# Optimization experiments

Measured on AMD Instinct MI355X. Metric: run time of the kernel, lower is better.

## Reference

```python
import jax, jax.numpy as jnp
import numpy as np
from jax import lax

NUM_IMG, NUM_HID, NUM_OUT = 3, 16, 10
NC = NUM_IMG + NUM_HID + NUM_OUT  # 29
HIDDEN = 128
FIRE_RATE = 0.5
LEAK = 0.01  # nn.LeakyReLU default negative_slope

_sobel_x = np.outer([1, 2, 1], [-1, 0, 1]) / 8.0
_sobel_y = _sobel_x.T

def _dw_kernel(k2d):
    # depthwise kernel, OIHW with feature_group_count=NC -> (NC, 1, 3, 3)
    k = jnp.asarray(k2d, dtype=jnp.float32)
    return jnp.tile(k[None, None], (NC, 1, 1, 1))

KSX = _dw_kernel(_sobel_x)
KSY = _dw_kernel(_sobel_y)

def _dwconv(x, k):
    # x: [B, NC, H, W]; zero padding=1 (F.conv2d default), groups=NC
    return lax.conv_general_dilated(x, k, window_strides=(1, 1),
                                    padding=((1, 1), (1, 1)),
                                    feature_group_count=NC,
                                    dimension_numbers=('NCHW', 'OIHW', 'NCHW'))

def _leaky(h):
    return jnp.where(h >= 0, h, LEAK * h)

def setup_inputs() -> dict:
    key = jax.random.key(0)
    k1, k2, k3, k4, kx = jax.random.split(key, 5)
    B, H, W = 16, 64, 64
    in_vec = NC * 3 + 1  # 29 channels x (identity + 2 sobel) + temporal = 88
    x = jax.random.uniform(kx, (B, NUM_IMG, H, W), dtype=jnp.float32)
    w1 = jax.random.normal(k1, (2 * HIDDEN, in_vec), dtype=jnp.float32) * 0.05
    b1 = jax.random.normal(k2, (2 * HIDDEN,), dtype=jnp.float32) * 0.05
    w2 = jax.random.normal(k3, (HIDDEN, 2 * HIDDEN), dtype=jnp.float32) * 0.05
    w3 = jax.random.normal(k4, (NC, HIDDEN), dtype=jnp.float32) * 0.02
    return {"x": x, "w1": w1, "b1": b1, "w2": w2, "w3": w3, "steps": 20}

def _nca_forward(x, w1, b1, w2, w3, steps):
    B, _, H, W = x.shape
    base_key = jax.random.key(42)
    # pad_input: zeros in hidden+output channels, then Gaussian noise N(0.5, 0.225) in hidden
    hid = 0.5 + 0.225 * jax.random.normal(jax.random.fold_in(base_key, 10_000),
                                          (B, NUM_HID, H, W), dtype=x.dtype)
    out = jnp.zeros((B, NUM_OUT, H, W), dtype=x.dtype)
    state = jnp.concatenate([x, hid, out], axis=1)  # [B, 29, H, W]
    # immutable image channels: zero dx on first NUM_IMG channels
    chan_mask = jnp.concatenate([jnp.zeros((NUM_IMG,), x.dtype),
                                 jnp.ones((NC - NUM_IMG,), x.dtype)])

    def step_fn(s, step):
        sx = _dwconv(s, KSX)
        sy = _dwconv(s, KSY)
        t = jnp.full((B, 1, H, W), 1.0, dtype=s.dtype) * (step.astype(s.dtype) / 100.0)
        perc = jnp.concatenate([s, sx, sy, t], axis=1)        # [B, 88, H, W]
        p = perc.transpose(0, 2, 3, 1)                         # [B, H, W, 88]
        h = _leaky(jnp.einsum('bhwi,oi->bhwo', p, w1) + b1)    # [B, H, W, 256]
        h = _leaky(jnp.einsum('bhwi,oi->bhwo', h, w2))         # [B, H, W, 128]
        dx = jnp.einsum('bhwi,oi->bhwo', h, w3)                # [B, H, W, 29]
        fire = jax.random.uniform(jax.random.fold_in(base_key, step),
                                  (B, H, W, 1), dtype=s.dtype) < FIRE_RATE
        dx = dx * fire.astype(s.dtype) * chan_mask             # stochastic + immutable mask
        s = s + dx.transpose(0, 3, 1, 2)
        return s, None

    state, _ = lax.scan(step_fn, state, jnp.arange(steps))
    # classify: mean-pool class channels over space, softmax
    class_ch = state[:, NUM_IMG + NUM_HID:, :, :]              # [B, 10, H, W]
    logits = jnp.mean(class_ch, axis=(2, 3))                   # [B, 10]
    return jax.nn.softmax(logits, axis=-1)

def reference(x, w1, b1, w2, w3, steps):
    return _nca_forward(x, w1, b1, w2, w3, steps)
```

## Files before the change

### kernel.cpp

```cpp
#include <hip/hip_runtime.h>


#define ROTL32(x, d) (((x) << (d)) | ((x) >> (32 - (d))))

struct U2 { unsigned a, b; };

__host__ __device__ inline U2 tf2x32(unsigned k0, unsigned k1, unsigned c0, unsigned c1) {
  unsigned ks2 = k0 ^ k1 ^ 0x1BD11BDAu;
  unsigned x0 = c0 + k0;
  unsigned x1 = c1 + k1;
#define TF_ROUND4(r0, r1, r2, r3)                                              \
  x0 += x1; x1 = ROTL32(x1, r0); x1 ^= x0;                                     \
  x0 += x1; x1 = ROTL32(x1, r1); x1 ^= x0;                                     \
  x0 += x1; x1 = ROTL32(x1, r2); x1 ^= x0;                                     \
  x0 += x1; x1 = ROTL32(x1, r3); x1 ^= x0;
  TF_ROUND4(13, 15, 26, 6)
  x0 += k1;  x1 += ks2 + 1u;
  TF_ROUND4(17, 29, 16, 24)
  x0 += ks2; x1 += k0 + 2u;
  TF_ROUND4(13, 15, 26, 6)
  x0 += k0;  x1 += k1 + 3u;
  TF_ROUND4(17, 29, 16, 24)
  x0 += k1;  x1 += ks2 + 4u;
  TF_ROUND4(13, 15, 26, 6)
  x0 += ks2; x1 += k0 + 5u;
#undef TF_ROUND4
  U2 r; r.a = x0; r.b = x1; return r;
}

__device__ inline float erfinv_xla(float x) {
  float w = -log1pf(-x * x);
  float p;
  if (w < 5.0f) {
    w -= 2.5f;
    p = 2.81022636e-08f;
    p = fmaf(p, w, 3.43273939e-07f);
    p = fmaf(p, w, -3.5233877e-06f);
    p = fmaf(p, w, -4.39150654e-06f);
    p = fmaf(p, w, 0.00021858087f);
    p = fmaf(p, w, -0.00125372503f);
    p = fmaf(p, w, -0.00417768164f);
    p = fmaf(p, w, 0.246640727f);
    p = fmaf(p, w, 1.50140941f);
  } else {
    w = sqrtf(w) - 3.0f;
    p = -0.000200214257f;
    p = fmaf(p, w, 0.000100950558f);
    p = fmaf(p, w, 0.00134934322f);
    p = fmaf(p, w, -0.00367342844f);
    p = fmaf(p, w, 0.00573950773f);
    p = fmaf(p, w, -0.0076224613f);
    p = fmaf(p, w, 0.00943887047f);
    p = fmaf(p, w, 1.00167406f);
    p = fmaf(p, w, 2.83297682f);
  }
  return p * x;
}

__device__ inline float leaky(float v) { return fmaxf(v, 0.01f * v); }

typedef __attribute__((ext_vector_type(8))) short bf16x8;
typedef __attribute__((ext_vector_type(4))) float f32x4;
typedef __attribute__((ext_vector_type(4))) unsigned int u32x4;

__host__ __device__ inline unsigned short bf16_rne(float x) {
  unsigned u = __float_as_uint(x);
  return (unsigned short)((u + 0x7FFFu + ((u >> 16) & 1u)) >> 16);
}

__device__ inline unsigned cvtpk(float a, float b) {
  unsigned r;
  asm("v_cvt_pk_bf16_f32 %0, %1, %2" : "=v"(r) : "v"(a), "v"(b));
  return r;
}

union Frag8 { u32x4 u; bf16x8 v; };

__device__ inline void split8(const float v[8], bf16x8& hi, bf16x8& lo) {
  Frag8 H, L;
#pragma unroll
  for (int j = 0; j < 8; j += 2) {
    unsigned p = cvtpk(v[j], v[j + 1]);
    H.u[j >> 1] = p;
    float r0 = v[j]     - __uint_as_float(p << 16);
    float r1 = v[j + 1] - __uint_as_float(p & 0xFFFF0000u);
    L.u[j >> 1] = cvtpk(r0, r1);
  }
  hi = H.v;
  lo = L.v;
}

__device__ inline int swz64(int m, int off) {
  int g = (off >> 4) ^ (m & 3);
  return (g << 4) | (off & 15);
}
__device__ inline int swz256(int m, int off) {
  int g = off >> 4;
  g = (g & ~7) | ((g ^ (m & 7)) & 7);
  return (g << 4) | (off & 15);
}

#define MFMA(a, b, c) __builtin_amdgcn_mfma_f32_16x16x32_bf16((a), (b), (c), 0, 0, 0)

__global__ void prep_weights(const float* __restrict__ w1, const float* __restrict__ w2,
                             const float* __restrict__ w3,
                             unsigned short* __restrict__ pw1,
                             unsigned short* __restrict__ pw2,
                             unsigned short* __restrict__ pw3) {
  int i = blockIdx.x * 256 + threadIdx.x;
  int e = i & 511, L = e >> 3, j = e & 7;
  int kq = (L >> 4) * 8 + j;
  int ln = L & 15;
  if (i < 96 * 512) {
    int tile = i >> 9;
    int f = tile & 3, kc = (tile >> 2) % 3, nc = tile / 12;
    int n = nc * 32 + (f >> 1) * 16 + ln;
    int src;
    if (kc == 0)      src = (kq < 29) ? kq : -1;
    else if (kc == 1) src = (kq < 29) ? 29 + kq : ((kq == 29) ? 87 : -1);
    else              src = (kq < 29) ? 58 + kq : -1;
    float v = (src >= 0) ? w1[n * 88 + src] : 0.0f;
    unsigned short h = bf16_rne(v);
    pw1[i] = (f & 1) ? bf16_rne(v - __uint_as_float(((unsigned)h) << 16)) : h;
  }
  if (i < 128 * 512) {
    int tile = i >> 9;
    int hl = tile & 1, t = (tile >> 1) & 7, nc = tile >> 4;
    int n = t * 16 + ln;
    int k = nc * 32 + kq;
    float v = w2[n * 256 + k];
    unsigned short h = bf16_rne(v);
    pw2[i] = hl ? bf16_rne(v - __uint_as_float(((unsigned)h) << 16)) : h;
  }
  if (i < 16 * 512) {
    int tile = i >> 9;
    int f = tile & 3, kc = tile >> 2;
    int n = (f >> 1) * 16 + ln;
    int k = kc * 32 + kq;
    float v = (n < 29) ? w3[n * 128 + k] : 0.0f;
    unsigned short h = bf16_rne(v);
    pw3[i] = (f & 1) ? bf16_rne(v - __uint_as_float(((unsigned)h) << 16)) : h;
  }
}

__global__ void init_state(const float* __restrict__ x, float* __restrict__ s0,
                           float* __restrict__ s1, unsigned hk0, unsigned hk1) {
  int idx = blockIdx.x * 256 + threadIdx.x;
  if (idx >= 16 * 29 * 4096) return;
  int pix = idx & 4095;
  int c = (idx >> 12) % 29;
  int b = idx / (4096 * 29);
  float v;
  if (c < 3) {
    v = x[(b * 3 + c) * 4096 + pix];
    s1[idx] = v;
  } else if (c < 19) {
    int ch = c - 3;
    int i = (b * 16 + ch) * 4096 + pix;
    const int half = 131072;
    unsigned bits;
    if (i < half) bits = tf2x32(hk0, hk1, (unsigned)i, (unsigned)(i + half)).a;
    else          bits = tf2x32(hk0, hk1, (unsigned)(i - half), (unsigned)i).b;
    float f = __uint_as_float((bits >> 9) | 0x3F800000u) - 1.0f;
    const float lo = -0x1.fffffep-1f;
    float u = fmaxf(lo, fmaf(f, 2.0f, lo));
    v = fmaf(0.225f, 1.41421356237f * erfinv_xla(u), 0.5f);
  } else {
    v = 0.0f;
  }
  s0[idx] = v;
}

__global__ __launch_bounds__(256, 2) void nca_step(
    const float* __restrict__ sin_, float* __restrict__ sout,
    const unsigned short* __restrict__ pw1, const float* __restrict__ b1,
    const unsigned short* __restrict__ pw2, const unsigned short* __restrict__ pw3,
    float tval, unsigned fk0, unsigned fk1) {
  __shared__ __align__(16) char lds[81920];
  char* h1h = lds;
  char* h1l = lds + 8192;
  char* h2h = lds + 16384;
  char* h2l = lds + 49152;
  float* sS = (float*)(lds + 16384);

  const int tid = threadIdx.x;
  const int w = tid >> 6;
  const int L = tid & 63;
  const int lane16 = L & 15;
  const int quad = L >> 4;
  const int b = blockIdx.z;
  const int ty0 = blockIdx.y * 8;
  const int tx0 = blockIdx.x * 16;
  const float* sb = sin_ + b * 29 * 4096;

  {
    float hv[21];
    int hix[21];
#pragma unroll
    for (int it = 0; it < 21; ++it) {
      int l = tid + it * 256;
      int c = l / 180;
      int rem = l - c * 180;
      int r = rem / 18;
      int x = rem - r * 18;
      int gy = ty0 - 1 + r, gx = tx0 - 1 + x;
      bool in = (l < 29 * 180);
      float v = 0.0f;
      if (in && (unsigned)gy < 64u && (unsigned)gx < 64u)
        v = sb[c * 4096 + gy * 64 + gx];
      hv[it] = v;
      hix[it] = in ? (c * 181 + r * 18 + x) : 5249;
    }
#pragma unroll
    for (int it = 0; it < 21; ++it) sS[hix[it]] = hv[it];
  }
  __syncthreads();

  const int am0 = w * 32 + lane16;
  const int am1 = w * 32 + 16 + lane16;
  bf16x8 a1h[2][3], a1l[2][3];
#pragma unroll
  for (int tt = 0; tt < 2; ++tt) {
    float vps[8], vpx[8], vpy[8];
#pragma unroll
    for (int j = 0; j < 8; ++j) {
      int c = quad * 8 + j;
      int cc = (c < 29) ? c : 0;
      const float* S = sS + cc * 181 + (2 * w + tt + 1) * 18 + (lane16 + 1);
      float m00 = S[-19], m01 = S[-18], m02 = S[-17];
      float m10 = S[-1],  m11 = S[0],   m12 = S[1];
      float m20 = S[17],  m21 = S[18],  m22 = S[19];
      bool valid = (c < 29);
      vps[j] = valid ? m11 : 0.0f;
      float px = ((m02 - m00) + 2.0f * (m12 - m10) + (m22 - m20)) * 0.125f;
      float py = ((m20 + 2.0f * m21 + m22) - (m00 + 2.0f * m01 + m02)) * 0.125f;
      vpx[j] = valid ? px : ((c == 29) ? tval : 0.0f);
      vpy[j] = valid ? py : 0.0f;
    }
    split8(vps, a1h[tt][0], a1l[tt][0]);
    split8(vpx, a1h[tt][1], a1l[tt][1]);
    split8(vpy, a1h[tt][2], a1l[tt][2]);
  }
  __syncthreads();

  const int L16 = L * 16;

  bf16x8 n1a, n1b, n1c, n1d;
  {
    const char* g = (const char*)pw1;
    n1a = *(const bf16x8*)(g + L16);
    n1b = *(const bf16x8*)(g + 1024 + L16);
    n1c = *(const bf16x8*)(g + 2048 + L16);
    n1d = *(const bf16x8*)(g + 3072 + L16);
  }

  float fire0, fire1;
  {
    int i0 = b * 4096 + (ty0 + 2 * w) * 64 + (tx0 + lane16);
    unsigned bits;
    if (i0 < 32768) bits = tf2x32(fk0, fk1, (unsigned)i0, (unsigned)(i0 + 32768)).a;
    else            bits = tf2x32(fk0, fk1, (unsigned)(i0 - 32768), (unsigned)i0).b;
    fire0 = (bits & 0x80000000u) ? 0.0f : 1.0f;
    int i1 = i0 + 64;
    if (i1 < 32768) bits = tf2x32(fk0, fk1, (unsigned)i1, (unsigned)(i1 + 32768)).a;
    else            bits = tf2x32(fk0, fk1, (unsigned)(i1 - 32768), (unsigned)i1).b;
    fire1 = (bits & 0x80000000u) ? 0.0f : 1.0f;
  }

  f32x4 acc2a[8], acc2b[8];
#pragma unroll
  for (int t = 0; t < 8; ++t) {
    acc2a[t] = (f32x4){0.f, 0.f, 0.f, 0.f};
    acc2b[t] = (f32x4){0.f, 0.f, 0.f, 0.f};
  }

#pragma unroll 1
  for (int nc = 0; nc < 8; ++nc) {
    f32x4 c0a = (f32x4){0.f, 0.f, 0.f, 0.f};
    f32x4 c1a = (f32x4){0.f, 0.f, 0.f, 0.f};
    f32x4 c0b = (f32x4){0.f, 0.f, 0.f, 0.f};
    f32x4 c1b = (f32x4){0.f, 0.f, 0.f, 0.f};
#pragma unroll
    for (int kc = 0; kc < 3; ++kc) {
      bf16x8 w1a = n1a, w1b = n1b, w1cc = n1c, w1d = n1d;
      {
        const int nt = (kc < 2) ? (nc * 3 + kc + 1) : (((nc + 1) & 7) * 3);
        const char* g = (const char*)pw1 + nt * 4096;
        n1a = *(const bf16x8*)(g + L16);
        n1b = *(const bf16x8*)(g + 1024 + L16);
        n1c = *(const bf16x8*)(g + 2048 + L16);
        n1d = *(const bf16x8*)(g + 3072 + L16);
      }
      __builtin_amdgcn_s_setprio(1);
      c0a = MFMA(a1h[0][kc], w1a, c0a);
      c1a = MFMA(a1h[0][kc], w1cc, c1a);
      c0b = MFMA(a1h[1][kc], w1a, c0b);
      c1b = MFMA(a1h[1][kc], w1cc, c1b);
      c0a = MFMA(a1h[0][kc], w1b, c0a);
      c1a = MFMA(a1h[0][kc], w1d, c1a);
      c0b = MFMA(a1h[1][kc], w1b, c0b);
      c1b = MFMA(a1h[1][kc], w1d, c1b);
      c0a = MFMA(a1l[0][kc], w1a, c0a);
      c1a = MFMA(a1l[0][kc], w1cc, c1a);
      c0b = MFMA(a1l[1][kc], w1a, c0b);
      c1b = MFMA(a1l[1][kc], w1cc, c1b);
      __builtin_amdgcn_s_setprio(0);
    }

    const char* g2 = (const char*)pw2 + nc * 16384;
    bf16x8 p0h = *(const bf16x8*)(g2 + L16);
    bf16x8 p0l = *(const bf16x8*)(g2 + 1024 + L16);
    bf16x8 p1h = *(const bf16x8*)(g2 + 2048 + L16);
    bf16x8 p1l = *(const bf16x8*)(g2 + 3072 + L16);

    float bv0 = b1[nc * 32 + lane16];
    float bv1 = b1[nc * 32 + 16 + lane16];
#pragma unroll
    for (int tt = 0; tt < 2; ++tt) {
      f32x4 cc0 = tt ? c0b : c0a;
      f32x4 cc1 = tt ? c1b : c1a;
#pragma unroll
      for (int r = 0; r < 4; ++r) {
        int m = w * 32 + tt * 16 + quad * 4 + r;
        float v0 = leaky(cc0[r] + bv0);
        float v1 = leaky(cc1[r] + bv1);
        unsigned ph = cvtpk(v0, v1);
        float r0 = v0 - __uint_as_float(ph << 16);
        float r1 = v1 - __uint_as_float(ph & 0xFFFF0000u);
        unsigned pl = cvtpk(r0, r1);
        *(unsigned short*)(h1h + m * 64 + swz64(m, lane16 * 2)) = (unsigned short)ph;
        *(unsigned short*)(h1h + m * 64 + swz64(m, 32 + lane16 * 2)) = (unsigned short)(ph >> 16);
        *(unsigned short*)(h1l + m * 64 + swz64(m, lane16 * 2)) = (unsigned short)pl;
        *(unsigned short*)(h1l + m * 64 + swz64(m, 32 + lane16 * 2)) = (unsigned short)(pl >> 16);
      }
    }
    bf16x8 ah0 = *(const bf16x8*)(h1h + am0 * 64 + swz64(am0, quad * 16));
    bf16x8 al0 = *(const bf16x8*)(h1l + am0 * 64 + swz64(am0, quad * 16));
    bf16x8 ah1 = *(const bf16x8*)(h1h + am1 * 64 + swz64(am1, quad * 16));
    bf16x8 al1 = *(const bf16x8*)(h1l + am1 * 64 + swz64(am1, quad * 16));
#pragma unroll
    for (int t = 0; t < 8; ++t) {
      bf16x8 bh = (t & 1) ? p1h : p0h;
      bf16x8 bl = (t & 1) ? p1l : p0l;
      if (t < 6) {
        const char* g = g2 + (t + 2) * 2048;
        if (t & 1) {
          p1h = *(const bf16x8*)(g + L16);
          p1l = *(const bf16x8*)(g + 1024 + L16);
        } else {
          p0h = *(const bf16x8*)(g + L16);
          p0l = *(const bf16x8*)(g + 1024 + L16);
        }
      }
      __builtin_amdgcn_s_setprio(1);
      acc2a[t] = MFMA(ah0, bh, acc2a[t]);
      acc2b[t] = MFMA(ah1, bh, acc2b[t]);
      acc2a[t] = MFMA(ah0, bl, acc2a[t]);
      acc2b[t] = MFMA(ah1, bl, acc2b[t]);
      acc2a[t] = MFMA(al0, bh, acc2a[t]);
      acc2b[t] = MFMA(al1, bh, acc2b[t]);
      __builtin_amdgcn_s_setprio(0);
    }
  }

#pragma unroll
  for (int tt = 0; tt < 2; ++tt) {
#pragma unroll
    for (int t = 0; t < 8; t += 2) {
#pragma unroll
      for (int r = 0; r < 4; ++r) {
        int m = w * 32 + tt * 16 + quad * 4 + r;
        float va = leaky(tt ? acc2b[t][r] : acc2a[t][r]);
        float vb = leaky(tt ? acc2b[t + 1][r] : acc2a[t + 1][r]);
        unsigned ph = cvtpk(va, vb);
        float ra = va - __uint_as_float(ph << 16);
        float rb = vb - __uint_as_float(ph & 0xFFFF0000u);
        unsigned pl = cvtpk(ra, rb);
        int offa = (t * 16 + lane16) * 2;
        int offb = ((t + 1) * 16 + lane16) * 2;
        *(unsigned short*)(h2h + m * 256 + swz256(m, offa)) = (unsigned short)ph;
        *(unsigned short*)(h2h + m * 256 + swz256(m, offb)) = (unsigned short)(ph >> 16);
        *(unsigned short*)(h2l + m * 256 + swz256(m, offa)) = (unsigned short)pl;
        *(unsigned short*)(h2l + m * 256 + swz256(m, offb)) = (unsigned short)(pl >> 16);
      }
    }
  }

  bf16x8 m0, m1, m2, m3;
  {
    const char* g = (const char*)pw3;
    m0 = *(const bf16x8*)(g + L16);
    m1 = *(const bf16x8*)(g + 1024 + L16);
    m2 = *(const bf16x8*)(g + 2048 + L16);
    m3 = *(const bf16x8*)(g + 3072 + L16);
  }
  f32x4 d0a = (f32x4){0.f, 0.f, 0.f, 0.f};
  f32x4 d1a = (f32x4){0.f, 0.f, 0.f, 0.f};
  f32x4 d0b = (f32x4){0.f, 0.f, 0.f, 0.f};
  f32x4 d1b = (f32x4){0.f, 0.f, 0.f, 0.f};
#pragma unroll
  for (int kc = 0; kc < 4; ++kc) {
    bf16x8 q0 = m0, q1 = m1, q2 = m2, q3 = m3;
    if (kc < 3) {
      const char* g = (const char*)pw3 + (kc + 1) * 4096;
      m0 = *(const bf16x8*)(g + L16);
      m1 = *(const bf16x8*)(g + 1024 + L16);
      m2 = *(const bf16x8*)(g + 2048 + L16);
      m3 = *(const bf16x8*)(g + 3072 + L16);
    }
    bf16x8 ah0 = *(const bf16x8*)(h2h + am0 * 256 + swz256(am0, kc * 64 + quad * 16));
    bf16x8 al0 = *(const bf16x8*)(h2l + am0 * 256 + swz256(am0, kc * 64 + quad * 16));
    bf16x8 ah1 = *(const bf16x8*)(h2h + am1 * 256 + swz256(am1, kc * 64 + quad * 16));
    bf16x8 al1 = *(const bf16x8*)(h2l + am1 * 256 + swz256(am1, kc * 64 + quad * 16));
    __builtin_amdgcn_s_setprio(1);
    d0a = MFMA(ah0, q0, d0a);
    d1a = MFMA(ah0, q2, d1a);
    d0b = MFMA(ah1, q0, d0b);
    d1b = MFMA(ah1, q2, d1b);
    d0a = MFMA(ah0, q1, d0a);
    d1a = MFMA(ah0, q3, d1a);
    d0b = MFMA(ah1, q1, d0b);
    d1b = MFMA(ah1, q3, d1b);
    d0a = MFMA(al0, q0, d0a);
    d1a = MFMA(al0, q2, d1a);
    d0b = MFMA(al1, q0, d0b);
    d1b = MFMA(al1, q2, d1b);
    __builtin_amdgcn_s_setprio(0);
  }

  float fr0[4], fr1[4];
#pragma unroll
  for (int r = 0; r < 4; ++r) {
    fr0[r] = __shfl(fire0, quad * 4 + r, 64);
    fr1[r] = __shfl(fire1, quad * 4 + r, 64);
  }
  int gxq = tx0 + quad * 4;
  float* ob = sout + b * 29 * 4096;
#pragma unroll
  for (int tt = 0; tt < 2; ++tt) {
    int gy = ty0 + 2 * w + tt;
#pragma unroll
    for (int t3 = 0; t3 < 2; ++t3) {
      int c = t3 * 16 + lane16;
      if (c >= 3 && c <= 28) {
        float4 so = *(const float4*)(sb + c * 4096 + gy * 64 + gxq);
        f32x4 d = tt ? (t3 ? d1b : d0b) : (t3 ? d1a : d0a);
        const float* fr = tt ? fr1 : fr0;
        float4 o;
        o.x = fmaf(fr[0], d[0], so.x);
        o.y = fmaf(fr[1], d[1], so.y);
        o.z = fmaf(fr[2], d[2], so.z);
        o.w = fmaf(fr[3], d[3], so.w);
        *(float4*)(ob + c * 4096 + gy * 64 + gxq) = o;
      }
    }
  }
}

__global__ __launch_bounds__(256) void reduce_ch(const float* __restrict__ s,
                                                 float* __restrict__ part) {
  int blk = blockIdx.x;
  int b = blk / 10, o = blk - b * 10;
  const float4* ch = (const float4*)(s + ((size_t)b * 29 + 19 + o) * 4096);
  int tid = threadIdx.x;
  float4 v0 = ch[tid];
  float4 v1 = ch[tid + 256];
  float4 v2 = ch[tid + 512];
  float4 v3 = ch[tid + 768];
  float p = ((v0.x + v0.y) + (v0.z + v0.w)) + ((v1.x + v1.y) + (v1.z + v1.w)) +
            ((v2.x + v2.y) + (v2.z + v2.w)) + ((v3.x + v3.y) + (v3.z + v3.w));
#pragma unroll
  for (int d = 32; d > 0; d >>= 1) p += __shfl_down(p, d, 64);
  __shared__ float red[4];
  if ((tid & 63) == 0) red[tid >> 6] = p;
  __syncthreads();
  if (tid == 0)
    part[blk] = ((red[0] + red[1]) + (red[2] + red[3])) * (1.0f / 4096.0f);
}

__global__ __launch_bounds__(64) void softmax10(const float* __restrict__ part,
                                                float* __restrict__ out) {
  int b = blockIdx.x;
  int o = threadIdx.x;
  float v = (o < 10) ? part[b * 10 + o] : -__builtin_inff();
  float m = v;
#pragma unroll
  for (int d = 8; d > 0; d >>= 1) m = fmaxf(m, __shfl_xor(m, d, 16));
  float e = (o < 10) ? __expf(v - m) : 0.0f;
  e = (o < 10) ? expf(v - m) : 0.0f;
  float sum = e;
#pragma unroll
  for (int d = 8; d > 0; d >>= 1) sum += __shfl_xor(sum, d, 16);
  if (o < 10) out[b * 10 + o] = e / sum;
}

extern "C" void kernel_launch(void* const* d_in, const int* in_sizes, int n_in,
                              void* d_out, int out_size, void* d_ws, size_t ws_size,
                              hipStream_t stream) {
  const float* x  = (const float*)d_in[0];
  const float* w1 = (const float*)d_in[1];
  const float* b1 = (const float*)d_in[2];
  const float* w2 = (const float*)d_in[3];
  const float* w3 = (const float*)d_in[4];
  const int STEPS = 20;

  const size_t STATE = (size_t)16 * 29 * 4096;
  float* ws = (float*)d_ws;
  float* s0 = ws;
  float* s1 = ws + STATE;
  unsigned short* pw1 = (unsigned short*)(ws + 2 * STATE);
  unsigned short* pw2 = pw1 + 96 * 512;
  unsigned short* pw3 = pw2 + 128 * 512;
  float* part = (float*)(pw3 + 16 * 512);
  (void)ws_size; (void)n_in; (void)in_sizes; (void)out_size;

  prep_weights<<<256, 256, 0, stream>>>(w1, w2, w3, pw1, pw2, pw3);

  U2 hk = tf2x32(0u, 42u, 0u, 10000u);
  init_state<<<(16 * 29 * 4096 + 255) / 256, 256, 0, stream>>>(x, s0, s1, hk.a, hk.b);

  for (int s = 0; s < STEPS; ++s) {
    U2 fk = tf2x32(0u, 42u, 0u, (unsigned)s);
    float tval = (float)s / 100.0f;
    const float* in = (s & 1) ? s1 : s0;
    float* out = (s & 1) ? s0 : s1;
    dim3 grid(4, 8, 16);
    nca_step<<<grid, 256, 0, stream>>>(in, out, pw1, b1, pw2, pw3, tval, fk.a, fk.b);
  }
  reduce_ch<<<160, 256, 0, stream>>>(s0, part);
  softmax10<<<16, 64, 0, stream>>>(part, (float*)d_out);
}
```

Before: 692.5 us.

## Double per-block tile to 16x16 pixels to amortize weight loads over more rows

Each block now processes a 16x16 pixel tile (4 row-tiles per wave instead of 2), so weight fragments loaded from global memory feed twice as many MFMAs. LDS grows to 128KB and launch bounds drop to one block per CU, and the grid halves to 256 blocks. This trades occupancy and halo overhead for more weight reuse, and it raises register pressure with 32 accumulator tiles per wave.

After: 843.3 us. 21.8% more time.

```diff
diff --git a/kernel.cpp b/kernel.cpp
--- a/kernel.cpp
+++ b/kernel.cpp
@@ -171,17 +171,17 @@
   s0[idx] = v;
 }
 
-__global__ __launch_bounds__(256, 2) void nca_step(
+__global__ __launch_bounds__(256, 1) void nca_step(
     const float* __restrict__ sin_, float* __restrict__ sout,
     const unsigned short* __restrict__ pw1, const float* __restrict__ b1,
     const unsigned short* __restrict__ pw2, const unsigned short* __restrict__ pw3,
     float tval, unsigned fk0, unsigned fk1) {
-  __shared__ __align__(16) char lds[81920];
-  char* h1h = lds;
-  char* h1l = lds + 8192;
-  char* h2h = lds + 16384;
-  char* h2l = lds + 49152;
-  float* sS = (float*)(lds + 16384);
+  __shared__ __align__(16) char lds[131072];
+  char* h2h = lds;
+  char* h2l = lds + 65536;
+  char* h1h = lds + 65536;
+  char* h1l = lds + 65536 + 16384;
+  float* sS = (float*)lds;
 
   const int tid = threadIdx.x;
   const int w = tid >> 6;
@@ -189,44 +189,63 @@
   const int lane16 = L & 15;
   const int quad = L >> 4;
   const int b = blockIdx.z;
-  const int ty0 = blockIdx.y * 8;
+  const int ty0 = blockIdx.y * 16;
   const int tx0 = blockIdx.x * 16;
   const float* sb = sin_ + b * 29 * 4096;
 
   {
-    float hv[21];
-    int hix[21];
-#pragma unroll
-    for (int it = 0; it < 21; ++it) {
+    float hv[19];
+    int hix[19];
+#pragma unroll
+    for (int it = 0; it < 19; ++it) {
       int l = tid + it * 256;
-      int c = l / 180;
-      int rem = l - c * 180;
+      int c = l / 324;
+      int rem = l - c * 324;
       int r = rem / 18;
       int x = rem - r * 18;
       int gy = ty0 - 1 + r, gx = tx0 - 1 + x;
-      bool in = (l < 29 * 180);
+      bool in = (l < 29 * 324);
       float v = 0.0f;
       if (in && (unsigned)gy < 64u && (unsigned)gx < 64u)
         v = sb[c * 4096 + gy * 64 + gx];
       hv[it] = v;
-      hix[it] = in ? (c * 181 + r * 18 + x) : 5249;
-    }
-#pragma unroll
-    for (int it = 0; it < 21; ++it) sS[hix[it]] = hv[it];
+      hix[it] = in ? (c * 325 + r * 18 + x) : 9425;
+    }
+#pragma unroll
+    for (int it = 0; it < 19; ++it) sS[hix[it]] = hv[it];
+  }
+  {
+    float hv[18];
+    int hix[18];
+#pragma unroll
+    for (int it = 0; it < 18; ++it) {
+      int l = tid + (19 + it) * 256;
+      int c = l / 324;
+      int rem = l - c * 324;
+      int r = rem / 18;
+      int x = rem - r * 18;
+      int gy = ty0 - 1 + r, gx = tx0 - 1 + x;
+      bool in = (l < 29 * 324);
+      float v = 0.0f;
+      if (in && (unsigned)gy < 64u && (unsigned)gx < 64u)
+        v = sb[c * 4096 + gy * 64 + gx];
+      hv[it] = v;
+      hix[it] = in ? (c * 325 + r * 18 + x) : 9425;
+    }
+#pragma unroll
+    for (int it = 0; it < 18; ++it) sS[hix[it]] = hv[it];
   }
   __syncthreads();
 
-  const int am0 = w * 32 + lane16;
-  const int am1 = w * 32 + 16 + lane16;
-  bf16x8 a1h[2][3], a1l[2][3];
-#pragma unroll
-  for (int tt = 0; tt < 2; ++tt) {
+  bf16x8 a1h[4][3], a1l[4][3];
+#pragma unroll
+  for (int tt = 0; tt < 4; ++tt) {
     float vps[8], vpx[8], vpy[8];
 #pragma unroll
     for (int j = 0; j < 8; ++j) {
       int c = quad * 8 + j;
       int cc = (c < 29) ? c : 0;
-      const float* S = sS + cc * 181 + (2 * w + tt + 1) * 18 + (lane16 + 1);
+      const float* S = sS + cc * 325 + (4 * w + tt + 1) * 18 + (lane16 + 1);
       float m00 = S[-19], m01 = S[-18], m02 = S[-17];
       float m10 = S[-1],  m11 = S[0],   m12 = S[1];
       float m20 = S[17],  m21 = S[18],  m22 = S[19];
@@ -244,6 +263,7 @@
   __syncthreads();
 
   const int L16 = L * 16;
+  const int am0 = w * 64 + lane16;
 
   bf16x8 n1a, n1b, n1c, n1d;
   {
@@ -254,32 +274,30 @@
     n1d = *(const bf16x8*)(g + 3072 + L16);
   }
 
-  float fire0, fire1;
-  {
-    int i0 = b * 4096 + (ty0 + 2 * w) * 64 + (tx0 + lane16);
+  float fire[4];
+#pragma unroll
+  for (int tt = 0; tt < 4; ++tt) {
+    int i = b * 4096 + (ty0 + 4 * w + tt) * 64 + (tx0 + lane16);
     unsigned bits;
-    if (i0 < 32768) bits = tf2x32(fk0, fk1, (unsigned)i0, (unsigned)(i0 + 32768)).a;
-    else            bits = tf2x32(fk0, fk1, (unsigned)(i0 - 32768), (unsigned)i0).b;
-    fire0 = (bits & 0x80000000u) ? 0.0f : 1.0f;
-    int i1 = i0 + 64;
-    if (i1 < 32768) bits = tf2x32(fk0, fk1, (unsigned)i1, (unsigned)(i1 + 32768)).a;
-    else            bits = tf2x32(fk0, fk1, (unsigned)(i1 - 32768), (unsigned)i1).b;
-    fire1 = (bits & 0x80000000u) ? 0.0f : 1.0f;
-  }
-
-  f32x4 acc2a[8], acc2b[8];
-#pragma unroll
-  for (int t = 0; t < 8; ++t) {
-    acc2a[t] = (f32x4){0.f, 0.f, 0.f, 0.f};
-    acc2b[t] = (f32x4){0.f, 0.f, 0.f, 0.f};
-  }
+    if (i < 32768) bits = tf2x32(fk0, fk1, (unsigned)i, (unsigned)(i + 32768)).a;
+    else           bits = tf2x32(fk0, fk1, (unsigned)(i - 32768), (unsigned)i).b;
+    fire[tt] = (bits & 0x80000000u) ? 0.0f : 1.0f;
+  }
+
+  f32x4 acc2[4][8];
+#pragma unroll
+  for (int tt = 0; tt < 4; ++tt)
+#pragma unroll
+    for (int t = 0; t < 8; ++t) acc2[tt][t] = (f32x4){0.f, 0.f, 0.f, 0.f};
 
 #pragma unroll 1
   for (int nc = 0; nc < 8; ++nc) {
-    f32x4 c0a = (f32x4){0.f, 0.f, 0.f, 0.f};
-    f32x4 c1a = (f32x4){0.f, 0.f, 0.f, 0.f};
-    f32x4 c0b = (f32x4){0.f, 0.f, 0.f, 0.f};
-    f32x4 c1b = (f32x4){0.f, 0.f, 0.f, 0.f};
+    f32x4 c0[4], c1[4];
+#pragma unroll
+    for (int tt = 0; tt < 4; ++tt) {
+      c0[tt] = (f32x4){0.f, 0.f, 0.f, 0.f};
+      c1[tt] = (f32x4){0.f, 0.f, 0.f, 0.f};
+    }
 #pragma unroll
     for (int kc = 0; kc < 3; ++kc) {
       bf16x8 w1a = n1a, w1b = n1b, w1cc = n1c, w1d = n1d;
@@ -292,18 +310,21 @@
         n1d = *(const bf16x8*)(g + 3072 + L16);
       }
       __builtin_amdgcn_s_setprio(1);
-      c0a = MFMA(a1h[0][kc], w1a, c0a);
-      c1a = MFMA(a1h[0][kc], w1cc, c1a);
-      c0b = MFMA(a1h[1][kc], w1a, c0b);
-      c1b = MFMA(a1h[1][kc], w1cc, c1b);
-      c0a = MFMA(a1h[0][kc], w1b, c0a);
-      c1a = MFMA(a1h[0][kc], w1d, c1a);
-      c0b = MFMA(a1h[1][kc], w1b, c0b);
-      c1b = MFMA(a1h[1][kc], w1d, c1b);
-      c0a = MFMA(a1l[0][kc], w1a, c0a);
-      c1a = MFMA(a1l[0][kc], w1cc, c1a);
-      c0b = MFMA(a1l[1][kc], w1a, c0b);
-      c1b = MFMA(a1l[1][kc], w1cc, c1b);
+#pragma unroll
+      for (int tt = 0; tt < 4; ++tt) {
+        c0[tt] = MFMA(a1h[tt][kc], w1a, c0[tt]);
+        c1[tt] = MFMA(a1h[tt][kc], w1cc, c1[tt]);
+      }
+#pragma unroll
+      for (int tt = 0; tt < 4; ++tt) {
+        c0[tt] = MFMA(a1h[tt][kc], w1b, c0[tt]);
+        c1[tt] = MFMA(a1h[tt][kc], w1d, c1[tt]);
+      }
+#pragma unroll
+      for (int tt = 0; tt < 4; ++tt) {
+        c0[tt] = MFMA(a1l[tt][kc], w1a, c0[tt]);
+        c1[tt] = MFMA(a1l[tt][kc], w1cc, c1[tt]);
+      }
       __builtin_amdgcn_s_setprio(0);
     }
 
@@ -316,14 +337,12 @@
     float bv0 = b1[nc * 32 + lane16];
     float bv1 = b1[nc * 32 + 16 + lane16];
 #pragma unroll
-    for (int tt = 0; tt < 2; ++tt) {
-      f32x4 cc0 = tt ? c0b : c0a;
-      f32x4 cc1 = tt ? c1b : c1a;
+    for (int tt = 0; tt < 4; ++tt) {
 #pragma unroll
       for (int r = 0; r < 4; ++r) {
-        int m = w * 32 + tt * 16 + quad * 4 + r;
-        float v0 = leaky(cc0[r] + bv0);
-        float v1 = leaky(cc1[r] + bv1);
+        int m = w * 64 + tt * 16 + quad * 4 + r;
+        float v0 = leaky(c0[tt][r] + bv0);
+        float v1 = leaky(c1[tt][r] + bv1);
         unsigned ph = cvtpk(v0, v1);
         float r0 = v0 - __uint_as_float(ph << 16);
         float r1 = v1 - __uint_as_float(ph & 0xFFFF0000u);
@@ -334,10 +353,13 @@
         *(unsigned short*)(h1l + m * 64 + swz64(m, 32 + lane16 * 2)) = (unsigned short)(pl >> 16);
       }
     }
-    bf16x8 ah0 = *(const bf16x8*)(h1h + am0 * 64 + swz64(am0, quad * 16));
-    bf16x8 al0 = *(const bf16x8*)(h1l + am0 * 64 + swz64(am0, quad * 16));
-    bf16x8 ah1 = *(const bf16x8*)(h1h + am1 * 64 + swz64(am1, quad * 16));
-    bf16x8 al1 = *(const bf16x8*)(h1l + am1 * 64 + swz64(am1, quad * 16));
+    bf16x8 ah[4], al[4];
+#pragma unroll
+    for (int tt = 0; tt < 4; ++tt) {
+      int am = am0 + tt * 16;
+      ah[tt] = *(const bf16x8*)(h1h + am * 64 + swz64(am, quad * 16));
+      al[tt] = *(const bf16x8*)(h1l + am * 64 + swz64(am, quad * 16));
+    }
 #pragma unroll
     for (int t = 0; t < 8; ++t) {
       bf16x8 bh = (t & 1) ? p1h : p0h;
@@ -353,25 +375,27 @@
         }
       }
       __builtin_amdgcn_s_setprio(1);
-      acc2a[t] = MFMA(ah0, bh, acc2a[t]);
-      acc2b[t] = MFMA(ah1, bh, acc2b[t]);
-      acc2a[t] = MFMA(ah0, bl, acc2a[t]);
-      acc2b[t] = MFMA(ah1, bl, acc2b[t]);
-      acc2a[t] = MFMA(al0, bh, acc2a[t]);
-      acc2b[t] = MFMA(al1, bh, acc2b[t]);
+#pragma unroll
+      for (int tt = 0; tt < 4; ++tt) acc2[tt][t] = MFMA(ah[tt], bh, acc2[tt][t]);
+#pragma unroll
+      for (int tt = 0; tt < 4; ++tt) acc2[tt][t] = MFMA(ah[tt], bl, acc2[tt][t]);
+#pragma unroll
+      for (int tt = 0; tt < 4; ++tt) acc2[tt][t] = MFMA(al[tt], bh, acc2[tt][t]);
       __builtin_amdgcn_s_setprio(0);
     }
   }
 
-#pragma unroll
-  for (int tt = 0; tt < 2; ++tt) {
+  __syncthreads();
+
+#pragma unroll
+  for (int tt = 0; tt < 4; ++tt) {
 #pragma unroll
     for (int t = 0; t < 8; t += 2) {
 #pragma unroll
       for (int r = 0; r < 4; ++r) {
-        int m = w * 32 + tt * 16 + quad * 4 + r;
-        float va = leaky(tt ? acc2b[t][r] : acc2a[t][r]);
-        float vb = leaky(tt ? acc2b[t + 1][r] : acc2a[t + 1][r]);
+        int m = w * 64 + tt * 16 + quad * 4 + r;
+        float va = leaky(acc2[tt][t][r]);
+        float vb = leaky(acc2[tt][t + 1][r]);
         unsigned ph = cvtpk(va, vb);
         float ra = va - __uint_as_float(ph << 16);
         float rb = vb - __uint_as_float(ph & 0xFFFF0000u);
@@ -394,10 +418,12 @@
     m2 = *(const bf16x8*)(g + 2048 + L16);
     m3 = *(const bf16x8*)(g + 3072 + L16);
   }
-  f32x4 d0a = (f32x4){0.f, 0.f, 0.f, 0.f};
-  f32x4 d1a = (f32x4){0.f, 0.f, 0.f, 0.f};
-  f32x4 d0b = (f32x4){0.f, 0.f, 0.f, 0.f};
-  f32x4 d1b = (f32x4){0.f, 0.f, 0.f, 0.f};
+  f32x4 d0[4], d1[4];
+#pragma unroll
+  for (int tt = 0; tt < 4; ++tt) {
+    d0[tt] = (f32x4){0.f, 0.f, 0.f, 0.f};
+    d1[tt] = (f32x4){0.f, 0.f, 0.f, 0.f};
+  }
 #pragma unroll
   for (int kc = 0; kc < 4; ++kc) {
     bf16x8 q0 = m0, q1 = m1, q2 = m2, q3 = m3;
@@ -408,44 +434,46 @@
       m2 = *(const bf16x8*)(g + 2048 + L16);
       m3 = *(const bf16x8*)(g + 3072 + L16);
     }
-    bf16x8 ah0 = *(const bf16x8*)(h2h + am0 * 256 + swz256(am0, kc * 64 + quad * 16));
-    bf16x8 al0 = *(const bf16x8*)(h2l + am0 * 256 + swz256(am0, kc * 64 + quad * 16));
-    bf16x8 ah1 = *(const bf16x8*)(h2h + am1 * 256 + swz256(am1, kc * 64 + quad * 16));
-    bf16x8 al1 = *(const bf16x8*)(h2l + am1 * 256 + swz256(am1, kc * 64 + quad * 16));
+    bf16x8 ah[4], al[4];
+#pragma unroll
+    for (int tt = 0; tt < 4; ++tt) {
+      int am = am0 + tt * 16;
+      ah[tt] = *(const bf16x8*)(h2h + am * 256 + swz256(am, kc * 64 + quad * 16));
+      al[tt] = *(const bf16x8*)(h2l + am * 256 + swz256(am, kc * 64 + quad * 16));
+    }
     __builtin_amdgcn_s_setprio(1);
-    d0a = MFMA(ah0, q0, d0a);
-    d1a = MFMA(ah0, q2, d1a);
-    d0b = MFMA(ah1, q0, d0b);
-    d1b = MFMA(ah1, q2, d1b);
-    d0a = MFMA(ah0, q1, d0a);
-    d1a = MFMA(ah0, q3, d1a);
-    d0b = MFMA(ah1, q1, d0b);
-    d1b = MFMA(ah1, q3, d1b);
-    d0a = MFMA(al0, q0, d0a);
-    d1a = MFMA(al0, q2, d1a);
-    d0b = MFMA(al1, q0, d0b);
-    d1b = MFMA(al1, q2, d1b);
+#pragma unroll
+    for (int tt = 0; tt < 4; ++tt) {
+      d0[tt] = MFMA(ah[tt], q0, d0[tt]);
+      d1[tt] = MFMA(ah[tt], q2, d1[tt]);
+    }
+#pragma unroll
+    for (int tt = 0; tt < 4; ++tt) {
+      d0[tt] = MFMA(ah[tt], q1, d0[tt]);
+      d1[tt] = MFMA(ah[tt], q3, d1[tt]);
+    }
+#pragma unroll
+    for (int tt = 0; tt < 4; ++tt) {
+      d0[tt] = MFMA(al[tt], q0, d0[tt]);
+      d1[tt] = MFMA(al[tt], q2, d1[tt]);
+    }
     __builtin_amdgcn_s_setprio(0);
   }
 
-  float fr0[4], fr1[4];
-#pragma unroll
-  for (int r = 0; r < 4; ++r) {
-    fr0[r] = __shfl(fire0, quad * 4 + r, 64);
-    fr1[r] = __shfl(fire1, quad * 4 + r, 64);
-  }
   int gxq = tx0 + quad * 4;
   float* ob = sout + b * 29 * 4096;
 #pragma unroll
-  for (int tt = 0; tt < 2; ++tt) {
-    int gy = ty0 + 2 * w + tt;
+  for (int tt = 0; tt < 4; ++tt) {
+    float fr[4];
+#pragma unroll
+    for (int r = 0; r < 4; ++r) fr[r] = __shfl(fire[tt], quad * 4 + r, 64);
+    int gy = ty0 + 4 * w + tt;
 #pragma unroll
     for (int t3 = 0; t3 < 2; ++t3) {
       int c = t3 * 16 + lane16;
       if (c >= 3 && c <= 28) {
         float4 so = *(const float4*)(sb + c * 4096 + gy * 64 + gxq);
-        f32x4 d = tt ? (t3 ? d1b : d0b) : (t3 ? d1a : d0a);
-        const float* fr = tt ? fr1 : fr0;
+        f32x4 d = t3 ? d1[tt] : d0[tt];
         float4 o;
         o.x = fmaf(fr[0], d[0], so.x);
         o.y = fmaf(fr[1], d[1], so.y);
@@ -486,8 +514,7 @@
   float m = v;
 #pragma unroll
   for (int d = 8; d > 0; d >>= 1) m = fmaxf(m, __shfl_xor(m, d, 16));
-  float e = (o < 10) ? __expf(v - m) : 0.0f;
-  e = (o < 10) ? expf(v - m) : 0.0f;
+  float e = (o < 10) ? expf(v - m) : 0.0f;
   float sum = e;
 #pragma unroll
   for (int d = 8; d > 0; d >>= 1) sum += __shfl_xor(sum, d, 16);
@@ -524,7 +551,7 @@
     float tval = (float)s / 100.0f;
     const float* in = (s & 1) ? s1 : s0;
     float* out = (s & 1) ? s0 : s1;
-    dim3 grid(4, 8, 16);
+    dim3 grid(4, 4, 16);
     nca_step<<<grid, 256, 0, stream>>>(in, out, pw1, b1, pw2, pw3, tval, fk.a, fk.b);
   }
   reduce_ch<<<160, 256, 0, stream>>>(s0, part);
```

## Stage W2 tiles through double-buffered LDS and fuse layer-2 output into layer-3 loop

Applied to the files above, without the earlier changes.

W2 weight tiles are now loaded cooperatively into a double-buffered LDS region, prefetched one chunk ahead, instead of each wave reading every fragment straight from global memory. Layer-3 now processes the layer-2 result in 64-wide K slices: each slice is converted to bf16 hi/lo and written into the small h1 buffer before its MFMAs. This removes the large h2 buffer and cuts LDS use from 80 KB to 56 KB, which could allow more blocks per CU. The cost is an extra __syncthreads per nc iteration and more LDS traffic, plus a swizzle change and a redundant expf removed in the softmax.

Result: slower. 715.3 us (+3.3%).

```diff
diff --git a/kernel.cpp b/kernel.cpp
--- a/kernel.cpp
+++ b/kernel.cpp
@@ -91,12 +91,7 @@
 }
 
 __device__ inline int swz64(int m, int off) {
-  int g = (off >> 4) ^ (m & 3);
-  return (g << 4) | (off & 15);
-}
-__device__ inline int swz256(int m, int off) {
-  int g = off >> 4;
-  g = (g & ~7) | ((g ^ (m & 7)) & 7);
+  int g = (off >> 4) ^ ((m >> 1) & 3);
   return (g << 4) | (off & 15);
 }
 
@@ -176,12 +171,10 @@
     const unsigned short* __restrict__ pw1, const float* __restrict__ b1,
     const unsigned short* __restrict__ pw2, const unsigned short* __restrict__ pw3,
     float tval, unsigned fk0, unsigned fk1) {
-  __shared__ __align__(16) char lds[81920];
+  __shared__ __align__(16) char lds[57344];
   char* h1h = lds;
   char* h1l = lds + 8192;
-  char* h2h = lds + 16384;
-  char* h2l = lds + 49152;
-  float* sS = (float*)(lds + 16384);
+  float* sS = (float*)lds;
 
   const int tid = threadIdx.x;
   const int w = tid >> 6;
@@ -192,6 +185,16 @@
   const int ty0 = blockIdx.y * 8;
   const int tx0 = blockIdx.x * 16;
   const float* sb = sin_ + b * 29 * 4096;
+  const int L16 = L * 16;
+
+  bf16x8 sgv[4];
+  int sgd[4];
+#pragma unroll
+  for (int i = 0; i < 4; ++i) {
+    int j = w * 4 + i;
+    sgv[i] = *(const bf16x8*)((const char*)pw2 + j * 1024 + L16);
+    sgd[i] = 24576 + j * 1024 + L16;
+  }
 
   {
     float hv[21];
@@ -241,9 +244,10 @@
     split8(vpx, a1h[tt][1], a1l[tt][1]);
     split8(vpy, a1h[tt][2], a1l[tt][2]);
   }
+
+#pragma unroll
+  for (int i = 0; i < 4; ++i) *(bf16x8*)(lds + sgd[i]) = sgv[i];
   __syncthreads();
-
-  const int L16 = L * 16;
 
   bf16x8 n1a, n1b, n1c, n1d;
   {
@@ -276,6 +280,18 @@
 
 #pragma unroll 1
   for (int nc = 0; nc < 8; ++nc) {
+    const char* s2 = lds + ((nc & 1) ? 40960 : 24576);
+    if (nc < 7) {
+      int nc2 = nc + 1;
+      int dstb = (nc2 & 1) ? 40960 : 24576;
+#pragma unroll
+      for (int i = 0; i < 4; ++i) {
+        int j = w * 4 + i;
+        sgv[i] = *(const bf16x8*)((const char*)pw2 + nc2 * 16384 + j * 1024 + L16);
+        sgd[i] = dstb + j * 1024 + L16;
+      }
+    }
+
     f32x4 c0a = (f32x4){0.f, 0.f, 0.f, 0.f};
     f32x4 c1a = (f32x4){0.f, 0.f, 0.f, 0.f};
     f32x4 c0b = (f32x4){0.f, 0.f, 0.f, 0.f};
@@ -307,12 +323,6 @@
       __builtin_amdgcn_s_setprio(0);
     }
 
-    const char* g2 = (const char*)pw2 + nc * 16384;
-    bf16x8 p0h = *(const bf16x8*)(g2 + L16);
-    bf16x8 p0l = *(const bf16x8*)(g2 + 1024 + L16);
-    bf16x8 p1h = *(const bf16x8*)(g2 + 2048 + L16);
-    bf16x8 p1l = *(const bf16x8*)(g2 + 3072 + L16);
-
     float bv0 = b1[nc * 32 + lane16];
     float bv1 = b1[nc * 32 + 16 + lane16];
 #pragma unroll
@@ -340,18 +350,8 @@
     bf16x8 al1 = *(const bf16x8*)(h1l + am1 * 64 + swz64(am1, quad * 16));
 #pragma unroll
     for (int t = 0; t < 8; ++t) {
-      bf16x8 bh = (t & 1) ? p1h : p0h;
-      bf16x8 bl = (t & 1) ? p1l : p0l;
-      if (t < 6) {
-        const char* g = g2 + (t + 2) * 2048;
-        if (t & 1) {
-          p1h = *(const bf16x8*)(g + L16);
-          p1l = *(const bf16x8*)(g + 1024 + L16);
-        } else {
-          p0h = *(const bf16x8*)(g + L16);
-          p0l = *(const bf16x8*)(g + 1024 + L16);
-        }
-      }
+      bf16x8 bh = *(const bf16x8*)(s2 + t * 2048 + L16);
+      bf16x8 bl = *(const bf16x8*)(s2 + t * 2048 + 1024 + L16);
       __builtin_amdgcn_s_setprio(1);
       acc2a[t] = MFMA(ah0, bh, acc2a[t]);
       acc2b[t] = MFMA(ah1, bh, acc2b[t]);
@@ -361,12 +361,39 @@
       acc2b[t] = MFMA(al1, bh, acc2b[t]);
       __builtin_amdgcn_s_setprio(0);
     }
-  }
-
-#pragma unroll
-  for (int tt = 0; tt < 2; ++tt) {
-#pragma unroll
-    for (int t = 0; t < 8; t += 2) {
+
+    if (nc < 7) {
+#pragma unroll
+      for (int i = 0; i < 4; ++i) *(bf16x8*)(lds + sgd[i]) = sgv[i];
+    }
+    __syncthreads();
+  }
+
+  bf16x8 m0, m1, m2, m3;
+  {
+    const char* g = (const char*)pw3;
+    m0 = *(const bf16x8*)(g + L16);
+    m1 = *(const bf16x8*)(g + 1024 + L16);
+    m2 = *(const bf16x8*)(g + 2048 + L16);
+    m3 = *(const bf16x8*)(g + 3072 + L16);
+  }
+  f32x4 d0a = (f32x4){0.f, 0.f, 0.f, 0.f};
+  f32x4 d1a = (f32x4){0.f, 0.f, 0.f, 0.f};
+  f32x4 d0b = (f32x4){0.f, 0.f, 0.f, 0.f};
+  f32x4 d1b = (f32x4){0.f, 0.f, 0.f, 0.f};
+#pragma unroll
+  for (int kc = 0; kc < 4; ++kc) {
+    bf16x8 q0 = m0, q1 = m1, q2 = m2, q3 = m3;
+    if (kc < 3) {
+      const char* g = (const char*)pw3 + (kc + 1) * 4096;
+      m0 = *(const bf16x8*)(g + L16);
+      m1 = *(const bf16x8*)(g + 1024 + L16);
+      m2 = *(const bf16x8*)(g + 2048 + L16);
+      m3 = *(const bf16x8*)(g + 3072 + L16);
+    }
+    const int t = 2 * kc;
+#pragma unroll
+    for (int tt = 0; tt < 2; ++tt) {
 #pragma unroll
       for (int r = 0; r < 4; ++r) {
         int m = w * 32 + tt * 16 + quad * 4 + r;
@@ -376,42 +403,16 @@
         float ra = va - __uint_as_float(ph << 16);
         float rb = vb - __uint_as_float(ph & 0xFFFF0000u);
         unsigned pl = cvtpk(ra, rb);
-        int offa = (t * 16 + lane16) * 2;
-        int offb = ((t + 1) * 16 + lane16) * 2;
-        *(unsigned short*)(h2h + m * 256 + swz256(m, offa)) = (unsigned short)ph;
-        *(unsigned short*)(h2h + m * 256 + swz256(m, offb)) = (unsigned short)(ph >> 16);
-        *(unsigned short*)(h2l + m * 256 + swz256(m, offa)) = (unsigned short)pl;
-        *(unsigned short*)(h2l + m * 256 + swz256(m, offb)) = (unsigned short)(pl >> 16);
+        *(unsigned short*)(h1h + m * 64 + swz64(m, lane16 * 2)) = (unsigned short)ph;
+        *(unsigned short*)(h1h + m * 64 + swz64(m, 32 + lane16 * 2)) = (unsigned short)(ph >> 16);
+        *(unsigned short*)(h1l + m * 64 + swz64(m, lane16 * 2)) = (unsigned short)pl;
+        *(unsigned short*)(h1l + m * 64 + swz64(m, 32 + lane16 * 2)) = (unsigned short)(pl >> 16);
       }
     }
-  }
-
-  bf16x8 m0, m1, m2, m3;
-  {
-    const char* g = (const char*)pw3;
-    m0 = *(const bf16x8*)(g + L16);
-    m1 = *(const bf16x8*)(g + 1024 + L16);
-    m2 = *(const bf16x8*)(g + 2048 + L16);
-    m3 = *(const bf16x8*)(g + 3072 + L16);
-  }
-  f32x4 d0a = (f32x4){0.f, 0.f, 0.f, 0.f};
-  f32x4 d1a = (f32x4){0.f, 0.f, 0.f, 0.f};
-  f32x4 d0b = (f32x4){0.f, 0.f, 0.f, 0.f};
-  f32x4 d1b = (f32x4){0.f, 0.f, 0.f, 0.f};
-#pragma unroll
-  for (int kc = 0; kc < 4; ++kc) {
-    bf16x8 q0 = m0, q1 = m1, q2 = m2, q3 = m3;
-    if (kc < 3) {
-      const char* g = (const char*)pw3 + (kc + 1) * 4096;
-      m0 = *(const bf16x8*)(g + L16);
-      m1 = *(const bf16x8*)(g + 1024 + L16);
-      m2 = *(const bf16x8*)(g + 2048 + L16);
-      m3 = *(const bf16x8*)(g + 3072 + L16);
-    }
-    bf16x8 ah0 = *(const bf16x8*)(h2h + am0 * 256 + swz256(am0, kc * 64 + quad * 16));
-    bf16x8 al0 = *(const bf16x8*)(h2l + am0 * 256 + swz256(am0, kc * 64 + quad * 16));
-    bf16x8 ah1 = *(const bf16x8*)(h2h + am1 * 256 + swz256(am1, kc * 64 + quad * 16));
-    bf16x8 al1 = *(const bf16x8*)(h2l + am1 * 256 + swz256(am1, kc * 64 + quad * 16));
+    bf16x8 ah0 = *(const bf16x8*)(h1h + am0 * 64 + swz64(am0, quad * 16));
+    bf16x8 al0 = *(const bf16x8*)(h1l + am0 * 64 + swz64(am0, quad * 16));
+    bf16x8 ah1 = *(const bf16x8*)(h1h + am1 * 64 + swz64(am1, quad * 16));
+    bf16x8 al1 = *(const bf16x8*)(h1l + am1 * 64 + swz64(am1, quad * 16));
     __builtin_amdgcn_s_setprio(1);
     d0a = MFMA(ah0, q0, d0a);
     d1a = MFMA(ah0, q2, d1a);
@@ -486,8 +487,7 @@
   float m = v;
 #pragma unroll
   for (int d = 8; d > 0; d >>= 1) m = fmaxf(m, __shfl_xor(m, d, 16));
-  float e = (o < 10) ? __expf(v - m) : 0.0f;
-  e = (o < 10) ? expf(v - m) : 0.0f;
+  float e = (o < 10) ? expf(v - m) : 0.0f;
   float sum = e;
 #pragma unroll
   for (int d = 8; d > 0; d >>= 1) sum += __shfl_xor(sum, d, 16);
```

## Stream layer-2 activations through small LDS buffer into layer-3 MFMAs

Applied to the files above, without the earlier changes.

Instead of writing the full 128-wide second hidden layer (hi/lo bf16 split) to a 64KB LDS region and then running the output projection, each 32-column chunk is converted, written into the reused 8KB h1 buffers and consumed right away by the layer-3 MFMAs. This cuts the kernel's shared memory from 80KB to about 21KB, and launch bounds are raised to allow 3 blocks per CU, with a retuned swizzle for the 64-byte rows. The cost is a tighter register budget and reliance on each wave reading only its own rows, since there is no barrier between chunk writes and reads. The softmax's redundant double exp is also removed.

New measurement: 994.5 us. 43.6% more time.

```diff
diff --git a/kernel.cpp b/kernel.cpp
--- a/kernel.cpp
+++ b/kernel.cpp
@@ -91,12 +91,7 @@
 }
 
 __device__ inline int swz64(int m, int off) {
-  int g = (off >> 4) ^ (m & 3);
-  return (g << 4) | (off & 15);
-}
-__device__ inline int swz256(int m, int off) {
-  int g = off >> 4;
-  g = (g & ~7) | ((g ^ (m & 7)) & 7);
+  int g = (off >> 4) ^ ((m >> 1) & 3);
   return (g << 4) | (off & 15);
 }
 
@@ -171,17 +166,15 @@
   s0[idx] = v;
 }
 
-__global__ __launch_bounds__(256, 2) void nca_step(
+__global__ __launch_bounds__(256, 3) void nca_step(
     const float* __restrict__ sin_, float* __restrict__ sout,
     const unsigned short* __restrict__ pw1, const float* __restrict__ b1,
     const unsigned short* __restrict__ pw2, const unsigned short* __restrict__ pw3,
     float tval, unsigned fk0, unsigned fk1) {
-  __shared__ __align__(16) char lds[81920];
+  __shared__ __align__(16) char lds[21504];
   char* h1h = lds;
   char* h1l = lds + 8192;
-  char* h2h = lds + 16384;
-  char* h2l = lds + 49152;
-  float* sS = (float*)(lds + 16384);
+  float* sS = (float*)lds;
 
   const int tid = threadIdx.x;
   const int w = tid >> 6;
@@ -363,10 +356,31 @@
     }
   }
 
-#pragma unroll
-  for (int tt = 0; tt < 2; ++tt) {
-#pragma unroll
-    for (int t = 0; t < 8; t += 2) {
+  bf16x8 m0, m1, m2, m3;
+  {
+    const char* g = (const char*)pw3;
+    m0 = *(const bf16x8*)(g + L16);
+    m1 = *(const bf16x8*)(g + 1024 + L16);
+    m2 = *(const bf16x8*)(g + 2048 + L16);
+    m3 = *(const bf16x8*)(g + 3072 + L16);
+  }
+  f32x4 d0a = (f32x4){0.f, 0.f, 0.f, 0.f};
+  f32x4 d1a = (f32x4){0.f, 0.f, 0.f, 0.f};
+  f32x4 d0b = (f32x4){0.f, 0.f, 0.f, 0.f};
+  f32x4 d1b = (f32x4){0.f, 0.f, 0.f, 0.f};
+#pragma unroll
+  for (int kc = 0; kc < 4; ++kc) {
+    bf16x8 q0 = m0, q1 = m1, q2 = m2, q3 = m3;
+    if (kc < 3) {
+      const char* g = (const char*)pw3 + (kc + 1) * 4096;
+      m0 = *(const bf16x8*)(g + L16);
+      m1 = *(const bf16x8*)(g + 1024 + L16);
+      m2 = *(const bf16x8*)(g + 2048 + L16);
+      m3 = *(const bf16x8*)(g + 3072 + L16);
+    }
+    const int t = 2 * kc;
+#pragma unroll
+    for (int tt = 0; tt < 2; ++tt) {
 #pragma unroll
       for (int r = 0; r < 4; ++r) {
         int m = w * 32 + tt * 16 + quad * 4 + r;
@@ -376,42 +390,16 @@
         float ra = va - __uint_as_float(ph << 16);
         float rb = vb - __uint_as_float(ph & 0xFFFF0000u);
         unsigned pl = cvtpk(ra, rb);
-        int offa = (t * 16 + lane16) * 2;
-        int offb = ((t + 1) * 16 + lane16) * 2;
-        *(unsigned short*)(h2h + m * 256 + swz256(m, offa)) = (unsigned short)ph;
-        *(unsigned short*)(h2h + m * 256 + swz256(m, offb)) = (unsigned short)(ph >> 16);
-        *(unsigned short*)(h2l + m * 256 + swz256(m, offa)) = (unsigned short)pl;
-        *(unsigned short*)(h2l + m * 256 + swz256(m, offb)) = (unsigned short)(pl >> 16);
+        *(unsigned short*)(h1h + m * 64 + swz64(m, lane16 * 2)) = (unsigned short)ph;
+        *(unsigned short*)(h1h + m * 64 + swz64(m, 32 + lane16 * 2)) = (unsigned short)(ph >> 16);
+        *(unsigned short*)(h1l + m * 64 + swz64(m, lane16 * 2)) = (unsigned short)pl;
+        *(unsigned short*)(h1l + m * 64 + swz64(m, 32 + lane16 * 2)) = (unsigned short)(pl >> 16);
       }
     }
-  }
-
-  bf16x8 m0, m1, m2, m3;
-  {
-    const char* g = (const char*)pw3;
-    m0 = *(const bf16x8*)(g + L16);
-    m1 = *(const bf16x8*)(g + 1024 + L16);
-    m2 = *(const bf16x8*)(g + 2048 + L16);
-    m3 = *(const bf16x8*)(g + 3072 + L16);
-  }
-  f32x4 d0a = (f32x4){0.f, 0.f, 0.f, 0.f};
-  f32x4 d1a = (f32x4){0.f, 0.f, 0.f, 0.f};
-  f32x4 d0b = (f32x4){0.f, 0.f, 0.f, 0.f};
-  f32x4 d1b = (f32x4){0.f, 0.f, 0.f, 0.f};
-#pragma unroll
-  for (int kc = 0; kc < 4; ++kc) {
-    bf16x8 q0 = m0, q1 = m1, q2 = m2, q3 = m3;
-    if (kc < 3) {
-      const char* g = (const char*)pw3 + (kc + 1) * 4096;
-      m0 = *(const bf16x8*)(g + L16);
-      m1 = *(const bf16x8*)(g + 1024 + L16);
-      m2 = *(const bf16x8*)(g + 2048 + L16);
-      m3 = *(const bf16x8*)(g + 3072 + L16);
-    }
-    bf16x8 ah0 = *(const bf16x8*)(h2h + am0 * 256 + swz256(am0, kc * 64 + quad * 16));
-    bf16x8 al0 = *(const bf16x8*)(h2l + am0 * 256 + swz256(am0, kc * 64 + quad * 16));
-    bf16x8 ah1 = *(const bf16x8*)(h2h + am1 * 256 + swz256(am1, kc * 64 + quad * 16));
-    bf16x8 al1 = *(const bf16x8*)(h2l + am1 * 256 + swz256(am1, kc * 64 + quad * 16));
+    bf16x8 ah0 = *(const bf16x8*)(h1h + am0 * 64 + swz64(am0, quad * 16));
+    bf16x8 al0 = *(const bf16x8*)(h1l + am0 * 64 + swz64(am0, quad * 16));
+    bf16x8 ah1 = *(const bf16x8*)(h1h + am1 * 64 + swz64(am1, quad * 16));
+    bf16x8 al1 = *(const bf16x8*)(h1l + am1 * 64 + swz64(am1, quad * 16));
     __builtin_amdgcn_s_setprio(1);
     d0a = MFMA(ah0, q0, d0a);
     d1a = MFMA(ah0, q2, d1a);
@@ -486,8 +474,7 @@
   float m = v;
 #pragma unroll
   for (int d = 8; d > 0; d >>= 1) m = fmaxf(m, __shfl_xor(m, d, 16));
-  float e = (o < 10) ? __expf(v - m) : 0.0f;
-  e = (o < 10) ? expf(v - m) : 0.0f;
+  float e = (o < 10) ? expf(v - m) : 0.0f;
   float sum = e;
 #pragma unroll
   for (int d = 8; d > 0; d >>= 1) sum += __shfl_xor(sum, d, 16);
```
